# Kernel optimization log

Hardware: AMD Instinct MI355X
Metric: run time of the kernel (lower is better)

## Reference

```python
import jax, jax.numpy as jnp
import numpy as np

B, D, H, C = 512, 1024, 512, 4


def setup_inputs() -> dict:
    key = jax.random.key(0)
    k_x, k_v, k_w = jax.random.split(key, 3)
    # x holds categorical values in [0, C) used as float multipliers
    x = jax.random.randint(k_x, (B, D), 0, C).astype(jnp.float32)
    # xavier_normal_ per torch fan computation: V fan_in=D*C, fan_out=H*C; W fan_in=D, fan_out=H
    V = jax.random.normal(k_v, (H, D, C), jnp.float32) * np.float32(np.sqrt(2.0 / (D * C + H * C)))
    b = jnp.zeros((D, C), jnp.float32)
    W = jax.random.normal(k_w, (H, D), jnp.float32) * np.float32(np.sqrt(2.0 / (D + H)))
    c = jnp.zeros((1, H), jnp.float32)
    return {"x": x, "V": V, "b": b, "W": W, "c": c}


def _nade_forward(x, V, b, W, c):
    Bsz = x.shape[0]
    a0 = jnp.broadcast_to(c, (Bsz, c.shape[1]))  # [B, H]
    # per-step slices stacked along leading D axis for lax.scan
    xs = (jnp.transpose(V, (1, 0, 2)),  # [D, H, C]
          b,                            # [D, C]
          W.T,                          # [D, H]
          x.T)                          # [D, B]

    def step(a, inp):
        V_d, b_d, w_d, x_d = inp
        h = jax.nn.sigmoid(a)                 # [B, H]
        logits = h @ V_d + b_d                # [B, C]
        p = jax.nn.log_softmax(logits, axis=1)
        a_new = a + x_d[:, None] * w_d[None, :]  # rank-1 update of running preactivation
        return a_new, (logits, p)

    _, (logits, p) = jax.lax.scan(step, a0, xs)   # each [D, B, C]
    y_hat = jnp.transpose(logits, (1, 0, 2)).reshape(Bsz, -1)  # [B, D*C], d-major blocks of size C
    p_hat = jnp.transpose(p, (1, 0, 2)).reshape(Bsz, -1)
    return y_hat, p_hat


def reference(x, V, b, W, c):
    return _nade_forward(x, V, b, W, c)
```

## Files before the change

kernel.cpp:

```cpp
#include <hip/hip_runtime.h>


#define Bv 512
#define Dv 1024
#define Hv 512
#define Cv 4
#define Kv 32
#define DCv 32

#define L2E 1.4426950408889634f
#define LN2 0.6931471805599453f

typedef __attribute__((ext_vector_type(8))) short short8;
typedef __attribute__((ext_vector_type(4))) float f32x4;

__device__ __forceinline__ float fexp2(float x) { return __builtin_amdgcn_exp2f(x); }
__device__ __forceinline__ float flog2(float x) { return __builtin_amdgcn_logf(x); }
__device__ __forceinline__ float frcp(float x)  { return __builtin_amdgcn_rcpf(x); }

__device__ __forceinline__ unsigned bf16pk(float lo, float hi) {
    return __builtin_amdgcn_perm(__float_as_uint(hi), __float_as_uint(lo), 0x07060302u);
}
__device__ __forceinline__ unsigned short bf16rne(float f) {
    unsigned u = __float_as_uint(f);
    return (unsigned short)((u + 0x7FFFu + ((u >> 16) & 1u)) >> 16);
}

__global__ __launch_bounds__(256) void k_prepW(const float* __restrict__ W,
                                               float* __restrict__ WtL) {
    __shared__ float t[64][65];
    const int tile = blockIdx.x;
    const int tr   = tile >> 4;
    const int tc   = tile & 15;
    const int lx = threadIdx.x & 15;
    const int ly = threadIdx.x >> 4;
#pragma unroll
    for (int r = 0; r < 64; r += 16) {
        int row = r + ly;
        float4 v = *(const float4*)(W + (size_t)(tr * 64 + row) * Dv + tc * 64 + lx * 4);
        t[row][lx * 4 + 0] = v.x;
        t[row][lx * 4 + 1] = v.y;
        t[row][lx * 4 + 2] = v.z;
        t[row][lx * 4 + 3] = v.w;
    }
    __syncthreads();
#pragma unroll
    for (int r = 0; r < 64; r += 16) {
        int row = r + ly;
        float4 o = make_float4(t[lx * 4 + 0][row] * L2E,
                               t[lx * 4 + 1][row] * L2E,
                               t[lx * 4 + 2][row] * L2E,
                               t[lx * 4 + 3][row] * L2E);
        *(float4*)(WtL + (size_t)(tc * 64 + row) * 512 + tr * 64 + lx * 4) = o;
    }
}

__global__ __launch_bounds__(512) void k_mid(
        const float* __restrict__ x, const float* __restrict__ V,
        const float* __restrict__ WtL,
        unsigned short* __restrict__ VtA4, float* __restrict__ xt,
        float* __restrict__ A0) {
    __shared__ __align__(16) char smem[16640];
    const int blk = blockIdx.x;

    if (blk < 2048) {
        float* xs = (float*)smem;
        const int k  = blk >> 6;
        const int bg = blk & 63;
        const int h  = threadIdx.x;
        const int d0 = k * DCv;
        if (threadIdx.x < DCv * 8) {
            int g = threadIdx.x >> 5;
            int j = threadIdx.x & 31;
            xs[j * 8 + g] = x[(size_t)(bg * 8 + g) * Dv + d0 + j];
        }
        __syncthreads();
        float acc[8];
#pragma unroll
        for (int g = 0; g < 8; ++g) acc[g] = 0.0f;
        const float* wp = WtL + (size_t)d0 * Hv + h;
        for (int j = 0; j < DCv; ++j) {
            float wv = wp[(size_t)j * Hv];
            const float4 x0 = *(const float4*)(xs + j * 8);
            const float4 x1 = *(const float4*)(xs + j * 8 + 4);
            acc[0] = fmaf(x0.x, wv, acc[0]);
            acc[1] = fmaf(x0.y, wv, acc[1]);
            acc[2] = fmaf(x0.z, wv, acc[2]);
            acc[3] = fmaf(x0.w, wv, acc[3]);
            acc[4] = fmaf(x1.x, wv, acc[4]);
            acc[5] = fmaf(x1.y, wv, acc[5]);
            acc[6] = fmaf(x1.z, wv, acc[6]);
            acc[7] = fmaf(x1.w, wv, acc[7]);
        }
#pragma unroll
        for (int g = 0; g < 8; ++g)
            A0[((size_t)k * Bv + bg * 8 + g) * Hv + h] = acc[g];
    } else if (blk < 2304) {
        unsigned short* tile = (unsigned short*)smem;
        const int d0  = (blk - 2048) * 4;
        const int dd  = threadIdx.x & 3;
        const int hb0 = threadIdx.x >> 2;
#pragma unroll
        for (int p = 0; p < 4; ++p) {
            int h = p * 128 + hb0;
            float4 v = *(const float4*)(V + ((size_t)h * Dv + d0 + dd) * Cv);
            int hb = h >> 5, q = (h >> 3) & 3, j = h & 7;
            int base = ((dd * 16 + hb) * 16 + q * 4) * 8 + j;
            tile[base + 0 * 8] = bf16rne(v.x);
            tile[base + 1 * 8] = bf16rne(v.y);
            tile[base + 2 * 8] = bf16rne(v.z);
            tile[base + 3 * 8] = bf16rne(v.w);
        }
        __syncthreads();
        uint4* dst = (uint4*)(VtA4 + (size_t)d0 * 2048);
        const uint4* srcp = (const uint4*)tile;
        for (int tt = threadIdx.x; tt < 1024; tt += 512) dst[tt] = srcp[tt];
    } else {
        float (*t)[65] = (float(*)[65])smem;
        const int tile = blk - 2304;
        const int tr   = tile >> 4;
        const int tc   = tile & 15;
        const int lx = threadIdx.x & 15;
        const int ly = threadIdx.x >> 4;
#pragma unroll
        for (int r = 0; r < 64; r += 32) {
            int row = r + ly;
            float4 v = *(const float4*)(x + (size_t)(tr * 64 + row) * Dv + tc * 64 + lx * 4);
            t[row][lx * 4 + 0] = v.x;
            t[row][lx * 4 + 1] = v.y;
            t[row][lx * 4 + 2] = v.z;
            t[row][lx * 4 + 3] = v.w;
        }
        __syncthreads();
#pragma unroll
        for (int r = 0; r < 64; r += 32) {
            int row = r + ly;
            float4 o = make_float4(t[lx * 4 + 0][row],
                                   t[lx * 4 + 1][row],
                                   t[lx * 4 + 2][row],
                                   t[lx * 4 + 3][row]);
            *(float4*)(xt + (size_t)(tc * 64 + row) * 512 + tr * 64 + lx * 4) = o;
        }
    }
}

__global__ void k_prefix(float* __restrict__ A0, const float* __restrict__ cbias) {
    int gid = blockIdx.x * blockDim.x + threadIdx.x;
    int h = gid & (Hv - 1);
    int bi = gid >> 9;
    float run = cbias[h] * L2E;
    float* p = A0 + (size_t)bi * Hv + h;
    for (int k = 0; k < Kv; ++k) {
        float t = p[(size_t)k * Bv * Hv];
        p[(size_t)k * Bv * Hv] = run;
        run += t;
    }
}

__global__ __launch_bounds__(256, 4) void k_main(
        const float* __restrict__ xt, const float* __restrict__ bbias,
        const unsigned short* __restrict__ VtA4, const float* __restrict__ WtL,
        const float* __restrict__ A0, float* __restrict__ out) {
    const int k    = blockIdx.x >> 5;
    const int bg   = blockIdx.x & 31;
    const int wid  = threadIdx.x >> 6;
    const int lane = threadIdx.x & 63;
    const int bl   = lane & 15;
    const int quad = lane >> 4;
    const int b    = bg * 16 + bl;
    const int d0   = k * DCv;

    __shared__ f32x4 red[2][8][4][16];

    float a[32];
    {
        const float* ap = A0 + ((size_t)k * Bv + b) * Hv + wid * 128 + quad * 8;
#pragma unroll
        for (int kb = 0; kb < 4; ++kb) {
            float4 t0 = *(const float4*)(ap + kb * 32);
            float4 t1 = *(const float4*)(ap + kb * 32 + 4);
            a[kb*8+0]=t0.x; a[kb*8+1]=t0.y; a[kb*8+2]=t0.z; a[kb*8+3]=t0.w;
            a[kb*8+4]=t1.x; a[kb*8+5]=t1.y; a[kb*8+6]=t1.z; a[kb*8+7]=t1.w;
        }
    }

    const bool act = (bl < 4);
    const unsigned short* vp = VtA4 + (((size_t)d0 * 16 + wid * 4) * 16 + quad * 4 + bl) * 8;
    const float* wp = WtL + (size_t)d0 * Hv + wid * 128 + quad * 8;
    const float* xp = xt + (size_t)d0 * Bv + b;

    const int  sE  = wid * 2 + (lane >> 5);
    const bool epi = ((lane >> 4) & 1) == 0;
    const float* bpE = bbias + (d0 + sE) * Cv;
    float* spY = out + (size_t)b * Dv * Cv + (d0 + sE) * Cv;
    float* spP = spY + (size_t)Bv * Dv * Cv;

    const short8 zfrag = {0,0,0,0,0,0,0,0};

    for (int i1 = 0; i1 < DCv / 8; ++i1) {
        const int buf = i1 & 1;
#pragma unroll 1
        for (int half = 0; half < 2; ++half) {
#pragma unroll
            for (int s = 0; s < 4; ++s) {
                short8 af[4];
#pragma unroll
                for (int kb = 0; kb < 4; ++kb)
                    af[kb] = act ? *(const short8*)(vp + s * 2048 + kb * 128) : zfrag;
                float xd = xp[s * Bv];

                unsigned pk[16];
#pragma unroll
                for (int m = 0; m < 32; m += 2) {
                    float s0 = frcp(1.0f + fexp2(-a[m]));
                    float s1 = frcp(1.0f + fexp2(-a[m + 1]));
                    pk[m >> 1] = bf16pk(s0, s1);
                }
                f32x4 acc = {0.f, 0.f, 0.f, 0.f};
#pragma unroll
                for (int kb = 0; kb < 4; ++kb) {
                    union { unsigned u[4]; short8 s8; } cv;
                    cv.u[0] = pk[kb*4+0]; cv.u[1] = pk[kb*4+1];
                    cv.u[2] = pk[kb*4+2]; cv.u[3] = pk[kb*4+3];
                    acc = __builtin_amdgcn_mfma_f32_16x16x32_bf16(af[kb], cv.s8, acc, 0, 0, 0);
                }
#pragma unroll
                for (int kb = 0; kb < 4; ++kb)
#pragma unroll
                    for (int j = 0; j < 8; ++j)
                        a[kb*8+j] = fmaf(xd, wp[s * Hv + kb*32 + j], a[kb*8+j]);

                if (quad == 0) red[buf][half * 4 + s][wid][bl] = acc;
            }
            vp += 4 * 2048;
            wp += 4 * Hv;
            xp += 4 * Bv;
        }
        __syncthreads();

        if (epi) {
            float4 bbv = *(const float4*)bpE;
            f32x4 r0 = red[buf][sE][0][bl];
            f32x4 r1 = red[buf][sE][1][bl];
            f32x4 r2 = red[buf][sE][2][bl];
            f32x4 r3 = red[buf][sE][3][bl];
            float w0 = r0.x + r1.x + r2.x + r3.x + bbv.x;
            float w1 = r0.y + r1.y + r2.y + r3.y + bbv.y;
            float w2 = r0.z + r1.z + r2.z + r3.z + bbv.z;
            float w3 = r0.w + r1.w + r2.w + r3.w + bbv.w;
            *(float4*)spY = make_float4(w0, w1, w2, w3);
            float mx = fmaxf(fmaxf(w0, w1), fmaxf(w2, w3));
            float e0 = fexp2((w0 - mx) * L2E);
            float e1 = fexp2((w1 - mx) * L2E);
            float e2 = fexp2((w2 - mx) * L2E);
            float e3 = fexp2((w3 - mx) * L2E);
            float lse = mx + flog2(e0 + e1 + e2 + e3) * LN2;
            *(float4*)spP = make_float4(w0 - lse, w1 - lse, w2 - lse, w3 - lse);
        }

        bpE += 8 * Cv;
        spY += 8 * Cv;
        spP += 8 * Cv;
    }
}

extern "C" void kernel_launch(void* const* d_in, const int* in_sizes, int n_in,
                              void* d_out, int out_size, void* d_ws, size_t ws_size,
                              hipStream_t stream) {
    const float* x  = (const float*)d_in[0];
    const float* V  = (const float*)d_in[1];
    const float* bb = (const float*)d_in[2];
    const float* W  = (const float*)d_in[3];
    const float* cb = (const float*)d_in[4];
    float* out = (float*)d_out;

    char* ws = (char*)d_ws;
    unsigned short* VtA4 = (unsigned short*)ws;
    float* WtL = (float*)(ws + (size_t)4 * 1024 * 1024);
    float* xt  = (float*)(ws + (size_t)6 * 1024 * 1024);
    float* A0  = (float*)(ws + (size_t)8 * 1024 * 1024);

    k_prepW<<<128, 256, 0, stream>>>(W, WtL);
    k_mid<<<2432, 512, 0, stream>>>(x, V, WtL, VtA4, xt, A0);
    k_prefix<<<(Bv * Hv) / 256, 256, 0, stream>>>(A0, cb);
    k_main<<<Kv * 32, 256, 0, stream>>>(xt, bb, VtA4, WtL, A0, out);
}
```

Measured before the change: 163.9 us.

## Fuse chunk partial sums with prefix scan and merge transpose prep kernels

The W and x transposes and the V bf16 repack are merged into one prep kernel, so launches go from four to three. The chunk partial-sum kernel now also does the exclusive prefix scan in registers while looping over all chunks, which removes the separate k_prefix pass that re-read and re-wrote A0. The main kernel's epilogue now runs every 16 steps with all lanes active instead of every 8 steps with half the lanes, which halves the __syncthreads count. The trade-off is that the fused prefix kernel launches only 128 blocks and walks the 32 chunks serially, so parallelism and GPU occupancy in that stage drop sharply.

```diff
diff --git a/kernel.cpp b/kernel.cpp
--- a/kernel.cpp
+++ b/kernel.cpp
@@ -26,50 +26,86 @@
     return (unsigned short)((u + 0x7FFFu + ((u >> 16) & 1u)) >> 16);
 }
 
-__global__ __launch_bounds__(256) void k_prepW(const float* __restrict__ W,
-                                               float* __restrict__ WtL) {
-    __shared__ float t[64][65];
-    const int tile = blockIdx.x;
-    const int tr   = tile >> 4;
-    const int tc   = tile & 15;
-    const int lx = threadIdx.x & 15;
-    const int ly = threadIdx.x >> 4;
-#pragma unroll
-    for (int r = 0; r < 64; r += 16) {
-        int row = r + ly;
-        float4 v = *(const float4*)(W + (size_t)(tr * 64 + row) * Dv + tc * 64 + lx * 4);
-        t[row][lx * 4 + 0] = v.x;
-        t[row][lx * 4 + 1] = v.y;
-        t[row][lx * 4 + 2] = v.z;
-        t[row][lx * 4 + 3] = v.w;
-    }
-    __syncthreads();
-#pragma unroll
-    for (int r = 0; r < 64; r += 16) {
-        int row = r + ly;
-        float4 o = make_float4(t[lx * 4 + 0][row] * L2E,
-                               t[lx * 4 + 1][row] * L2E,
-                               t[lx * 4 + 2][row] * L2E,
-                               t[lx * 4 + 3][row] * L2E);
-        *(float4*)(WtL + (size_t)(tc * 64 + row) * 512 + tr * 64 + lx * 4) = o;
-    }
-}
-
-__global__ __launch_bounds__(512) void k_mid(
-        const float* __restrict__ x, const float* __restrict__ V,
-        const float* __restrict__ WtL,
-        unsigned short* __restrict__ VtA4, float* __restrict__ xt,
-        float* __restrict__ A0) {
+__global__ __launch_bounds__(256) void k_prep2(
+        const float* __restrict__ W, const float* __restrict__ x,
+        const float* __restrict__ V,
+        float* __restrict__ WtL, float* __restrict__ xt,
+        unsigned short* __restrict__ VtA4) {
     __shared__ __align__(16) char smem[16640];
     const int blk = blockIdx.x;
 
-    if (blk < 2048) {
-        float* xs = (float*)smem;
-        const int k  = blk >> 6;
-        const int bg = blk & 63;
-        const int h  = threadIdx.x;
+    if (blk < 256) {
+        float (*t)[65] = (float(*)[65])smem;
+        const int mb   = blk >> 7;
+        const int tile = blk & 127;
+        const int tr   = tile >> 4;
+        const int tc   = tile & 15;
+        const float* src = mb ? x : W;
+        float* dst       = mb ? xt : WtL;
+        const float scale = mb ? 1.0f : L2E;
+        const int lx = threadIdx.x & 15;
+        const int ly = threadIdx.x >> 4;
+#pragma unroll
+        for (int r = 0; r < 64; r += 16) {
+            int row = r + ly;
+            float4 v = *(const float4*)(src + (size_t)(tr * 64 + row) * Dv + tc * 64 + lx * 4);
+            t[row][lx * 4 + 0] = v.x;
+            t[row][lx * 4 + 1] = v.y;
+            t[row][lx * 4 + 2] = v.z;
+            t[row][lx * 4 + 3] = v.w;
+        }
+        __syncthreads();
+#pragma unroll
+        for (int r = 0; r < 64; r += 16) {
+            int row = r + ly;
+            float4 o = make_float4(t[lx * 4 + 0][row] * scale,
+                                   t[lx * 4 + 1][row] * scale,
+                                   t[lx * 4 + 2][row] * scale,
+                                   t[lx * 4 + 3][row] * scale);
+            *(float4*)(dst + (size_t)(tc * 64 + row) * 512 + tr * 64 + lx * 4) = o;
+        }
+    } else {
+        unsigned short* tile = (unsigned short*)smem;
+        const int d0  = (blk - 256) * 4;
+        const int dd  = threadIdx.x & 3;
+        const int hb0 = threadIdx.x >> 2;
+#pragma unroll
+        for (int p = 0; p < 8; ++p) {
+            int h = p * 64 + hb0;
+            float4 v = *(const float4*)(V + ((size_t)h * Dv + d0 + dd) * Cv);
+            int hb = h >> 5, q = (h >> 3) & 3, j = h & 7;
+            int base = ((dd * 16 + hb) * 16 + q * 4) * 8 + j;
+            tile[base + 0 * 8] = bf16rne(v.x);
+            tile[base + 1 * 8] = bf16rne(v.y);
+            tile[base + 2 * 8] = bf16rne(v.z);
+            tile[base + 3 * 8] = bf16rne(v.w);
+        }
+        __syncthreads();
+        uint4* dst = (uint4*)(VtA4 + (size_t)d0 * 2048);
+        const uint4* srcp = (const uint4*)tile;
+        for (int tt = threadIdx.x; tt < 1024; tt += 256) dst[tt] = srcp[tt];
+    }
+}
+
+__global__ __launch_bounds__(256) void k_pp(
+        const float* __restrict__ x, const float* __restrict__ WtL,
+        const float* __restrict__ cbias, float* __restrict__ A0) {
+    __shared__ float xs[DCv * 8];
+    const int bg = blockIdx.x >> 1;
+    const int hs = blockIdx.x & 1;
+    const int h  = hs * 256 + threadIdx.x;
+
+    float run[8];
+    {
+        float cb = cbias[h] * L2E;
+#pragma unroll
+        for (int g = 0; g < 8; ++g) run[g] = cb;
+    }
+
+    for (int k = 0; k < Kv; ++k) {
         const int d0 = k * DCv;
-        if (threadIdx.x < DCv * 8) {
+        __syncthreads();
+        {
             int g = threadIdx.x >> 5;
             int j = threadIdx.x & 31;
             xs[j * 8 + g] = x[(size_t)(bg * 8 + g) * Dv + d0 + j];
@@ -79,6 +115,7 @@
 #pragma unroll
         for (int g = 0; g < 8; ++g) acc[g] = 0.0f;
         const float* wp = WtL + (size_t)d0 * Hv + h;
+#pragma unroll 4
         for (int j = 0; j < DCv; ++j) {
             float wv = wp[(size_t)j * Hv];
             const float4 x0 = *(const float4*)(xs + j * 8);
@@ -93,67 +130,10 @@
             acc[7] = fmaf(x1.w, wv, acc[7]);
         }
 #pragma unroll
-        for (int g = 0; g < 8; ++g)
-            A0[((size_t)k * Bv + bg * 8 + g) * Hv + h] = acc[g];
-    } else if (blk < 2304) {
-        unsigned short* tile = (unsigned short*)smem;
-        const int d0  = (blk - 2048) * 4;
-        const int dd  = threadIdx.x & 3;
-        const int hb0 = threadIdx.x >> 2;
-#pragma unroll
-        for (int p = 0; p < 4; ++p) {
-            int h = p * 128 + hb0;
-            float4 v = *(const float4*)(V + ((size_t)h * Dv + d0 + dd) * Cv);
-            int hb = h >> 5, q = (h >> 3) & 3, j = h & 7;
-            int base = ((dd * 16 + hb) * 16 + q * 4) * 8 + j;
-            tile[base + 0 * 8] = bf16rne(v.x);
-            tile[base + 1 * 8] = bf16rne(v.y);
-            tile[base + 2 * 8] = bf16rne(v.z);
-            tile[base + 3 * 8] = bf16rne(v.w);
-        }
-        __syncthreads();
-        uint4* dst = (uint4*)(VtA4 + (size_t)d0 * 2048);
-        const uint4* srcp = (const uint4*)tile;
-        for (int tt = threadIdx.x; tt < 1024; tt += 512) dst[tt] = srcp[tt];
-    } else {
-        float (*t)[65] = (float(*)[65])smem;
-        const int tile = blk - 2304;
-        const int tr   = tile >> 4;
-        const int tc   = tile & 15;
-        const int lx = threadIdx.x & 15;
-        const int ly = threadIdx.x >> 4;
-#pragma unroll
-        for (int r = 0; r < 64; r += 32) {
-            int row = r + ly;
-            float4 v = *(const float4*)(x + (size_t)(tr * 64 + row) * Dv + tc * 64 + lx * 4);
-            t[row][lx * 4 + 0] = v.x;
-            t[row][lx * 4 + 1] = v.y;
-            t[row][lx * 4 + 2] = v.z;
-            t[row][lx * 4 + 3] = v.w;
-        }
-        __syncthreads();
-#pragma unroll
-        for (int r = 0; r < 64; r += 32) {
-            int row = r + ly;
-            float4 o = make_float4(t[lx * 4 + 0][row],
-                                   t[lx * 4 + 1][row],
-                                   t[lx * 4 + 2][row],
-                                   t[lx * 4 + 3][row]);
-            *(float4*)(xt + (size_t)(tc * 64 + row) * 512 + tr * 64 + lx * 4) = o;
-        }
-    }
-}
-
-__global__ void k_prefix(float* __restrict__ A0, const float* __restrict__ cbias) {
-    int gid = blockIdx.x * blockDim.x + threadIdx.x;
-    int h = gid & (Hv - 1);
-    int bi = gid >> 9;
-    float run = cbias[h] * L2E;
-    float* p = A0 + (size_t)bi * Hv + h;
-    for (int k = 0; k < Kv; ++k) {
-        float t = p[(size_t)k * Bv * Hv];
-        p[(size_t)k * Bv * Hv] = run;
-        run += t;
+        for (int g = 0; g < 8; ++g) {
+            A0[((size_t)k * Bv + bg * 8 + g) * Hv + h] = run[g];
+            run[g] += acc[g];
+        }
     }
 }
 
@@ -170,7 +150,7 @@
     const int b    = bg * 16 + bl;
     const int d0   = k * DCv;
 
-    __shared__ f32x4 red[2][8][4][16];
+    __shared__ f32x4 red[2][16][4][16];
 
     float a[32];
     {
@@ -189,18 +169,12 @@
     const float* wp = WtL + (size_t)d0 * Hv + wid * 128 + quad * 8;
     const float* xp = xt + (size_t)d0 * Bv + b;
 
-    const int  sE  = wid * 2 + (lane >> 5);
-    const bool epi = ((lane >> 4) & 1) == 0;
-    const float* bpE = bbias + (d0 + sE) * Cv;
-    float* spY = out + (size_t)b * Dv * Cv + (d0 + sE) * Cv;
-    float* spP = spY + (size_t)Bv * Dv * Cv;
-
     const short8 zfrag = {0,0,0,0,0,0,0,0};
 
-    for (int i1 = 0; i1 < DCv / 8; ++i1) {
+    for (int i1 = 0; i1 < 2; ++i1) {
         const int buf = i1 & 1;
 #pragma unroll 1
-        for (int half = 0; half < 2; ++half) {
+        for (int q4 = 0; q4 < 4; ++q4) {
 #pragma unroll
             for (int s = 0; s < 4; ++s) {
                 short8 af[4];
@@ -230,7 +204,7 @@
                     for (int j = 0; j < 8; ++j)
                         a[kb*8+j] = fmaf(xd, wp[s * Hv + kb*32 + j], a[kb*8+j]);
 
-                if (quad == 0) red[buf][half * 4 + s][wid][bl] = acc;
+                if (quad == 0) red[buf][q4 * 4 + s][wid][bl] = acc;
             }
             vp += 4 * 2048;
             wp += 4 * Hv;
@@ -238,8 +212,10 @@
         }
         __syncthreads();
 
-        if (epi) {
-            float4 bbv = *(const float4*)bpE;
+        {
+            const int sE = wid * 4 + quad;
+            const int dd = d0 + i1 * 16 + sE;
+            float4 bbv = *(const float4*)(bbias + dd * Cv);
             f32x4 r0 = red[buf][sE][0][bl];
             f32x4 r1 = red[buf][sE][1][bl];
             f32x4 r2 = red[buf][sE][2][bl];
@@ -248,6 +224,8 @@
             float w1 = r0.y + r1.y + r2.y + r3.y + bbv.y;
             float w2 = r0.z + r1.z + r2.z + r3.z + bbv.z;
             float w3 = r0.w + r1.w + r2.w + r3.w + bbv.w;
+            float* spY = out + (size_t)b * Dv * Cv + (size_t)dd * Cv;
+            float* spP = spY + (size_t)Bv * Dv * Cv;
             *(float4*)spY = make_float4(w0, w1, w2, w3);
             float mx = fmaxf(fmaxf(w0, w1), fmaxf(w2, w3));
             float e0 = fexp2((w0 - mx) * L2E);
@@ -257,10 +235,6 @@
             float lse = mx + flog2(e0 + e1 + e2 + e3) * LN2;
             *(float4*)spP = make_float4(w0 - lse, w1 - lse, w2 - lse, w3 - lse);
         }
-
-        bpE += 8 * Cv;
-        spY += 8 * Cv;
-        spP += 8 * Cv;
     }
 }
 
@@ -280,8 +254,7 @@
     float* xt  = (float*)(ws + (size_t)6 * 1024 * 1024);
     float* A0  = (float*)(ws + (size_t)8 * 1024 * 1024);
 
-    k_prepW<<<128, 256, 0, stream>>>(W, WtL);
-    k_mid<<<2432, 512, 0, stream>>>(x, V, WtL, VtA4, xt, A0);
-    k_prefix<<<(Bv * Hv) / 256, 256, 0, stream>>>(A0, cb);
+    k_prep2<<<512, 256, 0, stream>>>(W, x, V, WtL, xt, VtA4);
+    k_pp<<<128, 256, 0, stream>>>(x, WtL, cb, A0);
     k_main<<<Kv * 32, 256, 0, stream>>>(xt, bb, VtA4, WtL, A0, out);
 }
```

Measured after the change: 232.4 us. 41.8% more time.

## Regroup prep kernels so prefix scan runs alongside V and x transposes

Applied to the files above, without the earlier changes.

The partial-sum GEMV moves into its own kernel, and the prefix scan over chunks is merged into one launch with the V bf16 repack and the x transpose. Those independent tasks now overlap instead of the scan running as a separate serial launch. Block size for the mixed kernel drops to 256, with the repack and transpose work split across more blocks. The launch count stays the same, and the gain depends on whether the smaller blocks and regrouping balance the work better.

```diff
diff --git a/kernel.cpp b/kernel.cpp
--- a/kernel.cpp
+++ b/kernel.cpp
@@ -55,75 +55,99 @@
     }
 }
 
-__global__ __launch_bounds__(512) void k_mid(
-        const float* __restrict__ x, const float* __restrict__ V,
-        const float* __restrict__ WtL,
-        unsigned short* __restrict__ VtA4, float* __restrict__ xt,
-        float* __restrict__ A0) {
+__global__ __launch_bounds__(512) void k_partial(const float* __restrict__ x,
+                          const float* __restrict__ WtL, float* __restrict__ A0) {
+    int k  = blockIdx.x >> 6;
+    int bg = blockIdx.x & 63;
+    int h  = threadIdx.x;
+    int d0 = k * DCv;
+
+    __shared__ float xs[DCv * 8];
+    if (threadIdx.x < DCv * 8) {
+        int g = threadIdx.x >> 5;
+        int j = threadIdx.x & 31;
+        xs[j * 8 + g] = x[(size_t)(bg * 8 + g) * Dv + d0 + j];
+    }
+    __syncthreads();
+
+    float acc[8];
+#pragma unroll
+    for (int g = 0; g < 8; ++g) acc[g] = 0.0f;
+
+    const float* wp = WtL + (size_t)d0 * Hv + h;
+    for (int j = 0; j < DCv; ++j) {
+        float wv = wp[(size_t)j * Hv];
+        const float4 x0 = *(const float4*)(xs + j * 8);
+        const float4 x1 = *(const float4*)(xs + j * 8 + 4);
+        acc[0] = fmaf(x0.x, wv, acc[0]);
+        acc[1] = fmaf(x0.y, wv, acc[1]);
+        acc[2] = fmaf(x0.z, wv, acc[2]);
+        acc[3] = fmaf(x0.w, wv, acc[3]);
+        acc[4] = fmaf(x1.x, wv, acc[4]);
+        acc[5] = fmaf(x1.y, wv, acc[5]);
+        acc[6] = fmaf(x1.z, wv, acc[6]);
+        acc[7] = fmaf(x1.w, wv, acc[7]);
+    }
+#pragma unroll
+    for (int g = 0; g < 8; ++g)
+        A0[((size_t)k * Bv + bg * 8 + g) * Hv + h] = acc[g];
+}
+
+__global__ __launch_bounds__(256) void k_mix(
+        float* __restrict__ A0, const float* __restrict__ cbias,
+        const float* __restrict__ V, unsigned short* __restrict__ VtA4,
+        const float* __restrict__ x, float* __restrict__ xt) {
     __shared__ __align__(16) char smem[16640];
     const int blk = blockIdx.x;
 
-    if (blk < 2048) {
-        float* xs = (float*)smem;
-        const int k  = blk >> 6;
-        const int bg = blk & 63;
-        const int h  = threadIdx.x;
-        const int d0 = k * DCv;
-        if (threadIdx.x < DCv * 8) {
-            int g = threadIdx.x >> 5;
-            int j = threadIdx.x & 31;
-            xs[j * 8 + g] = x[(size_t)(bg * 8 + g) * Dv + d0 + j];
-        }
-        __syncthreads();
-        float acc[8];
-#pragma unroll
-        for (int g = 0; g < 8; ++g) acc[g] = 0.0f;
-        const float* wp = WtL + (size_t)d0 * Hv + h;
-        for (int j = 0; j < DCv; ++j) {
-            float wv = wp[(size_t)j * Hv];
-            const float4 x0 = *(const float4*)(xs + j * 8);
-            const float4 x1 = *(const float4*)(xs + j * 8 + 4);
-            acc[0] = fmaf(x0.x, wv, acc[0]);
-            acc[1] = fmaf(x0.y, wv, acc[1]);
-            acc[2] = fmaf(x0.z, wv, acc[2]);
-            acc[3] = fmaf(x0.w, wv, acc[3]);
-            acc[4] = fmaf(x1.x, wv, acc[4]);
-            acc[5] = fmaf(x1.y, wv, acc[5]);
-            acc[6] = fmaf(x1.z, wv, acc[6]);
-            acc[7] = fmaf(x1.w, wv, acc[7]);
-        }
-#pragma unroll
-        for (int g = 0; g < 8; ++g)
-            A0[((size_t)k * Bv + bg * 8 + g) * Hv + h] = acc[g];
-    } else if (blk < 2304) {
+    if (blk < 1024) {
+        int gid = blk * 256 + threadIdx.x;
+        int h = gid & (Hv - 1);
+        int bi = gid >> 9;
+        float run = cbias[h] * L2E;
+        float* p = A0 + (size_t)bi * Hv + h;
+        for (int k = 0; k < Kv; ++k) {
+            float t = p[(size_t)k * Bv * Hv];
+            p[(size_t)k * Bv * Hv] = run;
+            run += t;
+        }
+    } else if (blk < 2048) {
         unsigned short* tile = (unsigned short*)smem;
-        const int d0  = (blk - 2048) * 4;
+        const int vb = blk - 1024;
+        const int d0 = (vb >> 2) * 4;
+        const int hq = vb & 3;
         const int dd  = threadIdx.x & 3;
         const int hb0 = threadIdx.x >> 2;
 #pragma unroll
-        for (int p = 0; p < 4; ++p) {
-            int h = p * 128 + hb0;
+        for (int p = 0; p < 2; ++p) {
+            int h = hq * 128 + p * 64 + hb0;
             float4 v = *(const float4*)(V + ((size_t)h * Dv + d0 + dd) * Cv);
-            int hb = h >> 5, q = (h >> 3) & 3, j = h & 7;
-            int base = ((dd * 16 + hb) * 16 + q * 4) * 8 + j;
+            int hbl = (h >> 5) - hq * 4;
+            int q = (h >> 3) & 3, j = h & 7;
+            int base = (dd * 4 + hbl) * 128 + q * 32 + j;
             tile[base + 0 * 8] = bf16rne(v.x);
             tile[base + 1 * 8] = bf16rne(v.y);
             tile[base + 2 * 8] = bf16rne(v.z);
             tile[base + 3 * 8] = bf16rne(v.w);
         }
         __syncthreads();
-        uint4* dst = (uint4*)(VtA4 + (size_t)d0 * 2048);
-        const uint4* srcp = (const uint4*)tile;
-        for (int tt = threadIdx.x; tt < 1024; tt += 512) dst[tt] = srcp[tt];
+        {
+            const uint4* srcp = (const uint4*)tile;
+            int tt  = threadIdx.x;
+            int dd2 = tt >> 6;
+            int off = tt & 63;
+            uint4* dst = (uint4*)VtA4;
+            dst[(size_t)(d0 + dd2) * 256 + hq * 64 + off] = srcp[dd2 * 64 + off];
+        }
     } else {
         float (*t)[65] = (float(*)[65])smem;
-        const int tile = blk - 2304;
+        const int tile = blk - 2048;
         const int tr   = tile >> 4;
         const int tc   = tile & 15;
         const int lx = threadIdx.x & 15;
         const int ly = threadIdx.x >> 4;
 #pragma unroll
-        for (int r = 0; r < 64; r += 32) {
+        for (int r = 0; r < 64; r += 16) {
             int row = r + ly;
             float4 v = *(const float4*)(x + (size_t)(tr * 64 + row) * Dv + tc * 64 + lx * 4);
             t[row][lx * 4 + 0] = v.x;
@@ -133,7 +157,7 @@
         }
         __syncthreads();
 #pragma unroll
-        for (int r = 0; r < 64; r += 32) {
+        for (int r = 0; r < 64; r += 16) {
             int row = r + ly;
             float4 o = make_float4(t[lx * 4 + 0][row],
                                    t[lx * 4 + 1][row],
@@ -141,19 +165,6 @@
                                    t[lx * 4 + 3][row]);
             *(float4*)(xt + (size_t)(tc * 64 + row) * 512 + tr * 64 + lx * 4) = o;
         }
-    }
-}
-
-__global__ void k_prefix(float* __restrict__ A0, const float* __restrict__ cbias) {
-    int gid = blockIdx.x * blockDim.x + threadIdx.x;
-    int h = gid & (Hv - 1);
-    int bi = gid >> 9;
-    float run = cbias[h] * L2E;
-    float* p = A0 + (size_t)bi * Hv + h;
-    for (int k = 0; k < Kv; ++k) {
-        float t = p[(size_t)k * Bv * Hv];
-        p[(size_t)k * Bv * Hv] = run;
-        run += t;
     }
 }
 
@@ -281,7 +292,7 @@
     float* A0  = (float*)(ws + (size_t)8 * 1024 * 1024);
 
     k_prepW<<<128, 256, 0, stream>>>(W, WtL);
-    k_mid<<<2432, 512, 0, stream>>>(x, V, WtL, VtA4, xt, A0);
-    k_prefix<<<(Bv * Hv) / 256, 256, 0, stream>>>(A0, cb);
+    k_partial<<<Kv * (Bv / 8), 512, 0, stream>>>(x, WtL, A0);
+    k_mix<<<2176, 256, 0, stream>>>(A0, cb, V, VtA4, x, xt);
     k_main<<<Kv * 32, 256, 0, stream>>>(xt, bb, VtA4, WtL, A0, out);
 }
```

Result: no change. 165.0 us (+0.6%).
